# Performance work log

Measured on AMD Instinct MI355X. Metric: run time of the kernel, lower is better.

Reference implementation:

```python
import jax, jax.numpy as jnp
import numpy as np

DIM = 768
NUM_HEADS = 16
HEAD_DIM = DIM // NUM_HEADS  # 48
SCALE = 1.0 / np.sqrt(HEAD_DIM).astype(np.float32)


def setup_inputs() -> dict:
    key = jax.random.key(0)
    k1, k2, k3 = jax.random.split(key, 3)
    B, S = 4, 2048
    x = jax.random.normal(k1, (B, S, DIM), dtype=jnp.float32)
    # nn.Linear(dim, 3*dim, bias=False): weight stored transposed -> use [in, out]
    w_qkv = jax.random.normal(k2, (DIM, 3 * DIM), dtype=jnp.float32) * (1.0 / np.sqrt(DIM))
    w_proj = jax.random.normal(k3, (DIM, DIM), dtype=jnp.float32) * (1.0 / np.sqrt(DIM))
    b_proj = jnp.zeros((DIM,), dtype=jnp.float32)
    return {"x": x, "w_qkv": w_qkv, "w_proj": w_proj, "b_proj": b_proj}


def reference(x, w_qkv, w_proj, b_proj):
    B, S, D = x.shape
    qkv = x @ w_qkv                                   # [B,S,3D]
    qkv = qkv.reshape(B, S, 3, NUM_HEADS, HEAD_DIM)
    q, k, v = jnp.moveaxis(qkv, 2, 0)                 # each [B,S,H,hd]
    q = q.transpose(0, 2, 1, 3)                       # [B,H,S,hd]
    k = k.transpose(0, 2, 1, 3)
    v = v.transpose(0, 2, 1, 3)
    attn = jnp.einsum('bhqd,bhkd->bhqk', q, k) * SCALE
    attn = jax.nn.softmax(attn, axis=-1)              # dropout: identity (eval mode)
    out = jnp.einsum('bhqk,bhkd->bhqd', attn, v)      # [B,H,S,hd]
    out = out.transpose(0, 2, 1, 3).reshape(B, S, D)
    return out @ w_proj + b_proj
```

## Files before the change

kernel.cpp:

```cpp
#include <hip/hip_runtime.h>
#include <hip/hip_bf16.h>

#define DIMD   768
#define HEADS  16
#define HD     48
#define SEQ    2048
#define BATCH  4
#define NTOK   (BATCH * SEQ)
#define QKVD   (3 * DIMD)

typedef __attribute__((ext_vector_type(8)))  short s16x8;
typedef __attribute__((ext_vector_type(4)))  float f32x4;
typedef __attribute__((ext_vector_type(16))) float f32x16;
typedef unsigned short ushort_t;

static __device__ __forceinline__ unsigned short f2b(float f) {
  union { __hip_bfloat16 b; unsigned short s; } u;
  u.b = __float2bfloat16(f);
  return u.s;
}
static __device__ __forceinline__ float b2f(unsigned short v) {
  union { float f; unsigned u; } x;
  x.u = ((unsigned)v) << 16;
  return x.f;
}
static __device__ __forceinline__ unsigned pk2(float a, float b) {
  return (unsigned)f2b(a) | ((unsigned)f2b(b) << 16);
}

static __device__ __forceinline__ void gload_lds16(const void* g, void* l) {
  __builtin_amdgcn_global_load_lds(
      (const __attribute__((address_space(1))) unsigned int*)g,
      (__attribute__((address_space(3))) unsigned int*)l, 16, 0, 0);
}

__global__ __launch_bounds__(256) void cvt_bf16(const float* __restrict__ in,
                                                ushort_t* __restrict__ out, int n8) {
  int i = blockIdx.x * 256 + threadIdx.x;
  if (i >= n8) return;
  float4 a = ((const float4*)in)[i * 2];
  float4 b = ((const float4*)in)[i * 2 + 1];
  s16x8 v;
  v[0] = (short)f2b(a.x); v[1] = (short)f2b(a.y);
  v[2] = (short)f2b(a.z); v[3] = (short)f2b(a.w);
  v[4] = (short)f2b(b.x); v[5] = (short)f2b(b.y);
  v[6] = (short)f2b(b.z); v[7] = (short)f2b(b.w);
  ((s16x8*)out)[i] = v;
}

__global__ __launch_bounds__(256) void tcvt_bf16(const float* __restrict__ in,
                                                 ushort_t* __restrict__ out,
                                                 int R, int C) {
  __shared__ float T[32][33];
  const int c0 = blockIdx.x * 32, r0 = blockIdx.y * 32;
  const int lc = threadIdx.x & 31, lr = threadIdx.x >> 5;
#pragma unroll
  for (int i = 0; i < 4; ++i)
    T[lr + 8 * i][lc] = in[(size_t)(r0 + lr + 8 * i) * C + c0 + lc];
  __syncthreads();
#pragma unroll
  for (int i = 0; i < 4; ++i)
    out[(size_t)(c0 + lr + 8 * i) * R + r0 + lc] = f2b(T[lc][lr + 8 * i]);
}

template <int OUT_BF16>
__global__ __launch_bounds__(256) void gemm_bf16(
    const ushort_t* __restrict__ A, const ushort_t* __restrict__ Bt,
    const float* __restrict__ bias, void* __restrict__ Cout,
    int M, int N, int K) {
  __shared__ __align__(16) ushort_t As[128 * 64];
  __shared__ __align__(16) ushort_t Bs[128 * 64];

  const int tid = threadIdx.x;
  const int lane = tid & 63;
  const int w = tid >> 6;
  const int m0 = blockIdx.y * 128, n0 = blockIdx.x * 128;
  const int wm = (w >> 1) * 64, wn = (w & 1) * 64;

  const int c16s = (tid & 7) ^ ((tid >> 3) & 7);
  const ushort_t* aSrc = A + (size_t)(m0 + (tid >> 3)) * K + c16s * 8;
  const ushort_t* bSrc = Bt + (size_t)(n0 + (tid >> 3)) * K + c16s * 8;

  f32x4 acc[4][4];
#pragma unroll
  for (int i = 0; i < 4; ++i)
#pragma unroll
    for (int j = 0; j < 4; ++j) {
      acc[i][j][0] = 0.f; acc[i][j][1] = 0.f;
      acc[i][j][2] = 0.f; acc[i][j][3] = 0.f;
    }

  for (int k0 = 0; k0 < K; k0 += 64) {
    __syncthreads();
#pragma unroll
    for (int r = 0; r < 4; ++r) {
      gload_lds16(aSrc + (size_t)(r * 32) * K + k0,
                  (char*)As + (r * 256 + w * 64) * 16);
      gload_lds16(bSrc + (size_t)(r * 32) * K + k0,
                  (char*)Bs + (r * 256 + w * 64) * 16);
    }
    __syncthreads();

#pragma unroll
    for (int ks = 0; ks < 2; ++ks) {
      s16x8 af[4], bfr[4];
#pragma unroll
      for (int i = 0; i < 4; ++i) {
        const int ar = wm + i * 16 + (lane & 15);
        const int ac = (ks * 4 + (lane >> 4)) ^ (ar & 7);
        af[i] = *(const s16x8*)&As[ar * 64 + ac * 8];
        const int br = wn + i * 16 + (lane & 15);
        const int bc = (ks * 4 + (lane >> 4)) ^ (br & 7);
        bfr[i] = *(const s16x8*)&Bs[br * 64 + bc * 8];
      }
#pragma unroll
      for (int i = 0; i < 4; ++i)
#pragma unroll
        for (int j = 0; j < 4; ++j)
          acc[i][j] = __builtin_amdgcn_mfma_f32_16x16x32_bf16(
              af[i], bfr[j], acc[i][j], 0, 0, 0);
    }
  }

  if (OUT_BF16) {
    ushort_t* C = (ushort_t*)Cout;
#pragma unroll
    for (int i = 0; i < 4; ++i)
#pragma unroll
      for (int j = 0; j < 4; ++j) {
        const int col = n0 + wn + j * 16 + (lane & 15);
#pragma unroll
        for (int r = 0; r < 4; ++r) {
          const int row = m0 + wm + i * 16 + (lane >> 4) * 4 + r;
          C[(size_t)row * N + col] = f2b(acc[i][j][r]);
        }
      }
  } else {
    float* C = (float*)Cout;
#pragma unroll
    for (int i = 0; i < 4; ++i)
#pragma unroll
      for (int j = 0; j < 4; ++j) {
        const int col = n0 + wn + j * 16 + (lane & 15);
        const float bv = bias ? bias[col] : 0.f;
#pragma unroll
        for (int r = 0; r < 4; ++r) {
          const int row = m0 + wm + i * 16 + (lane >> 4) * 4 + r;
          C[(size_t)row * N + col] = acc[i][j][r] + bv;
        }
      }
  }
}

#define KVB 64
#define QPW 32
#define QPB 256
#define NT  (SEQ / KVB)

__global__ __launch_bounds__(512) void attn_mfma(const ushort_t* __restrict__ QKV,
                                                 ushort_t* __restrict__ Aout) {
  const int bh = blockIdx.x;
  const int qt = blockIdx.y;
  const int b = bh >> 4, h = bh & 15;
  const int tid  = threadIdx.x;
  const int w    = tid >> 6;
  const int lane = tid & 63;
  const int l31  = lane & 31;
  const int hi   = lane >> 5;

  __shared__ __align__(16) ushort_t Kfrag[6 * 64 * 8];
  __shared__ __align__(16) ushort_t Vt[64 * 64];

  if (tid < 240) *(uint2*)&Vt[49 * 64 + tid * 4] = make_uint2(0u, 0u);
  if (tid < 64) Vt[48 * 64 + tid] = (ushort_t)0x3F80;

  const ushort_t* qkv_b = QKV + (size_t)b * SEQ * QKVD;

  const float qs = 0.14433756729740643f * 1.44269504088896340f;
  const int qrow = qt * QPB + w * QPW + l31;
  const ushort_t* qsrc = qkv_b + (size_t)qrow * QKVD + h * HD;
  s16x8 qf[3];
#pragma unroll
  for (int ks = 0; ks < 3; ++ks) {
    s16x8 raw = *(const s16x8*)(qsrc + ks * 16 + hi * 8);
    s16x8 v;
#pragma unroll
    for (int j = 0; j < 8; ++j) v[j] = (short)f2b(b2f((unsigned short)raw[j]) * qs);
    qf[ks] = v;
  }

  f32x16 o[2];
#pragma unroll
  for (int mt = 0; mt < 2; ++mt)
#pragma unroll
    for (int r = 0; r < 16; ++r) o[mt][r] = 0.f;

  const int srow = lane;
  const int g0 = w;
  const ushort_t* kv0 = qkv_b + (size_t)srow * QKVD + DIMD + h * HD;

  s16x8 ka, va;
  auto loadKV = [&](int kt) {
    if (g0 < 6) {
      const ushort_t* base = kv0 + (size_t)(kt * KVB) * QKVD;
      ka = *(const s16x8*)(base + g0 * 8);
      va = *(const s16x8*)(base + DIMD + g0 * 8);
    }
  };
  auto writeKV = [&]() {
    if (g0 < 6) {
      const int slot = (srow >> 5) * 3 + (g0 >> 1);
      const int pos = (((srow & 31) + ((g0 & 1) << 5)) ^ slot);
      *(s16x8*)&Kfrag[(slot * 64 + pos) * 8] = ka;
#pragma unroll
      for (int j = 0; j < 8; ++j)
        Vt[(8 * g0 + j) * 64 + (srow ^ (j << 3))] = (ushort_t)va[j];
    }
  };

  loadKV(0);

  for (int kt = 0; kt < NT; ++kt) {
    __syncthreads();
    writeKV();
    __syncthreads();
    if (kt + 1 < NT) loadKV(kt + 1);

    f32x16 s0, s1;
#pragma unroll
    for (int r = 0; r < 16; ++r) { s0[r] = 0.f; s1[r] = 0.f; }
    __builtin_amdgcn_s_setprio(1);
#pragma unroll
    for (int ks = 0; ks < 3; ++ks) {
      s16x8 a0 = *(const s16x8*)&Kfrag[(ks * 64 + (lane ^ ks)) * 8];
      s0 = __builtin_amdgcn_mfma_f32_32x32x16_bf16(a0, qf[ks], s0, 0, 0, 0);
      s16x8 a1 = *(const s16x8*)&Kfrag[((3 + ks) * 64 + (lane ^ (3 + ks))) * 8];
      s1 = __builtin_amdgcn_mfma_f32_32x32x16_bf16(a1, qf[ks], s1, 0, 0, 0);
    }
    __builtin_amdgcn_s_setprio(0);

    unsigned pw0[8], pw1[8];
#pragma unroll
    for (int g = 0; g < 8; ++g) {
      pw0[g] = pk2(__builtin_amdgcn_exp2f(s0[2 * g]),
                   __builtin_amdgcn_exp2f(s0[2 * g + 1]));
      pw1[g] = pk2(__builtin_amdgcn_exp2f(s1[2 * g]),
                   __builtin_amdgcn_exp2f(s1[2 * g + 1]));
    }

    __builtin_amdgcn_s_setprio(1);
#pragma unroll
    for (int ks = 0; ks < 4; ++ks) {
      unsigned w0 = (ks < 2) ? pw0[4 * (ks & 1) + 0] : pw1[4 * (ks & 1) + 0];
      unsigned w1 = (ks < 2) ? pw0[4 * (ks & 1) + 1] : pw1[4 * (ks & 1) + 1];
      unsigned w2 = (ks < 2) ? pw0[4 * (ks & 1) + 2] : pw1[4 * (ks & 1) + 2];
      unsigned w3 = (ks < 2) ? pw0[4 * (ks & 1) + 3] : pw1[4 * (ks & 1) + 3];
      asm("v_permlane32_swap_b32 %0, %1" : "+v"(w0), "+v"(w2));
      asm("v_permlane32_swap_b32 %0, %1" : "+v"(w1), "+v"(w3));
      union { unsigned u[4]; s16x8 v; } pf;
      pf.u[0] = w0; pf.u[1] = w1; pf.u[2] = w2; pf.u[3] = w3;
      const int keyb = ks * 16 + hi * 8;
#pragma unroll
      for (int mt = 0; mt < 2; ++mt) {
        const int hd = mt * 32 + l31;
        s16x8 vfrag = *(const s16x8*)&Vt[hd * 64 + (keyb ^ ((hd & 7) << 3))];
        o[mt] = __builtin_amdgcn_mfma_f32_32x32x16_bf16(vfrag, pf.v, o[mt], 0, 0, 0);
      }
    }
    __builtin_amdgcn_s_setprio(0);
  }

  const float lsum = __shfl(o[1][8], l31, 64);
  const float inv = 1.f / lsum;
  const int token = qt * QPB + w * QPW + l31;
  ushort_t* dst = Aout + ((size_t)b * SEQ + token) * DIMD + h * HD;
#pragma unroll
  for (int rq = 0; rq < 4; ++rq) {
    const int hd0 = 8 * rq + 4 * hi;
    uint2 pk;
    pk.x = pk2(o[0][4 * rq + 0] * inv, o[0][4 * rq + 1] * inv);
    pk.y = pk2(o[0][4 * rq + 2] * inv, o[0][4 * rq + 3] * inv);
    *(uint2*)(dst + hd0) = pk;
  }
#pragma unroll
  for (int rq = 0; rq < 2; ++rq) {
    const int hd0 = 32 + 8 * rq + 4 * hi;
    uint2 pk;
    pk.x = pk2(o[1][4 * rq + 0] * inv, o[1][4 * rq + 1] * inv);
    pk.y = pk2(o[1][4 * rq + 2] * inv, o[1][4 * rq + 3] * inv);
    *(uint2*)(dst + hd0) = pk;
  }
}

extern "C" void kernel_launch(void* const* d_in, const int* in_sizes, int n_in,
                              void* d_out, int out_size, void* d_ws, size_t ws_size,
                              hipStream_t stream) {
  const float* x      = (const float*)d_in[0];
  const float* w_qkv  = (const float*)d_in[1];
  const float* w_proj = (const float*)d_in[2];
  const float* b_proj = (const float*)d_in[3];
  float* out = (float*)d_out;

  ushort_t* xb     = (ushort_t*)d_ws;
  ushort_t* wqkvT  = xb + (size_t)NTOK * DIMD;
  ushort_t* wprojT = wqkvT + (size_t)QKVD * DIMD;
  ushort_t* qkv    = wprojT + (size_t)DIMD * DIMD;
  ushort_t* att    = qkv + (size_t)NTOK * QKVD;

  cvt_bf16<<<(NTOK * DIMD / 8 + 255) / 256, 256, 0, stream>>>(x, xb, NTOK * DIMD / 8);
  tcvt_bf16<<<dim3(QKVD / 32, DIMD / 32), 256, 0, stream>>>(w_qkv, wqkvT, DIMD, QKVD);
  tcvt_bf16<<<dim3(DIMD / 32, DIMD / 32), 256, 0, stream>>>(w_proj, wprojT, DIMD, DIMD);

  gemm_bf16<1><<<dim3(QKVD / 128, NTOK / 128), 256, 0, stream>>>(
      xb, wqkvT, nullptr, qkv, NTOK, QKVD, DIMD);

  attn_mfma<<<dim3(BATCH * HEADS, SEQ / QPB), 512, 0, stream>>>(qkv, att);

  gemm_bf16<0><<<dim3(DIMD / 128, NTOK / 128), 256, 0, stream>>>(
      att, wprojT, b_proj, out, NTOK, DIMD, DIMD);
}
```

Baseline: 151.5 us.

## Split attention KV loop across two blocks and merge partials in a new kernel

The attention grid gains a third dimension that divides the key/value sequence into two halves, so twice as many blocks run concurrently. Each block writes unnormalized fp16 partial outputs and its row sums to workspace. A new merge kernel adds the two partials and divides by the combined sum before producing the bf16 attention output. This targets low occupancy in the attention kernel, at the cost of extra global traffic, one more launch, and the risk of fp16 overflow or precision loss in the unnormalized partials.

New measurement: 162.7 us. +7.5%, slower.

```diff
diff --git a/kernel.cpp b/kernel.cpp
--- a/kernel.cpp
+++ b/kernel.cpp
@@ -1,5 +1,6 @@
 #include <hip/hip_runtime.h>
 #include <hip/hip_bf16.h>
+#include <hip/hip_fp16.h>
 
 #define DIMD   768
 #define HEADS  16
@@ -26,6 +27,19 @@
 }
 static __device__ __forceinline__ unsigned pk2(float a, float b) {
   return (unsigned)f2b(a) | ((unsigned)f2b(b) << 16);
+}
+static __device__ __forceinline__ unsigned short f2h(float f) {
+  union { __half h; unsigned short s; } u;
+  u.h = __float2half(f);
+  return u.s;
+}
+static __device__ __forceinline__ float h2f(unsigned short s) {
+  union { __half h; unsigned short s; } u;
+  u.s = s;
+  return __half2float(u.h);
+}
+static __device__ __forceinline__ unsigned pk2h(float a, float b) {
+  return (unsigned)f2h(a) | ((unsigned)f2h(b) << 16);
 }
 
 static __device__ __forceinline__ void gload_lds16(const void* g, void* l) {
@@ -156,11 +170,14 @@
 #define QPW 32
 #define QPB 256
 #define NT  (SEQ / KVB)
+#define NTS (NT / 2)
 
 __global__ __launch_bounds__(512) void attn_mfma(const ushort_t* __restrict__ QKV,
-                                                 ushort_t* __restrict__ Aout) {
+                                                 ushort_t* __restrict__ Opart,
+                                                 float* __restrict__ Lpart) {
   const int bh = blockIdx.x;
   const int qt = blockIdx.y;
+  const int ks_split = blockIdx.z;
   const int b = bh >> 4, h = bh & 15;
   const int tid  = threadIdx.x;
   const int w    = tid >> 6;
@@ -218,13 +235,14 @@
     }
   };
 
-  loadKV(0);
-
-  for (int kt = 0; kt < NT; ++kt) {
+  const int kt0 = ks_split * NTS;
+  loadKV(kt0);
+
+  for (int it = 0; it < NTS; ++it) {
     __syncthreads();
     writeKV();
     __syncthreads();
-    if (kt + 1 < NT) loadKV(kt + 1);
+    if (it + 1 < NTS) loadKV(kt0 + it + 1);
 
     f32x16 s0, s1;
 #pragma unroll
@@ -270,26 +288,52 @@
     __builtin_amdgcn_s_setprio(0);
   }
 
-  const float lsum = __shfl(o[1][8], l31, 64);
-  const float inv = 1.f / lsum;
   const int token = qt * QPB + w * QPW + l31;
-  ushort_t* dst = Aout + ((size_t)b * SEQ + token) * DIMD + h * HD;
+  const size_t tokg = (size_t)ks_split * NTOK + (size_t)b * SEQ + token;
+  ushort_t* dst = Opart + tokg * DIMD + h * HD;
 #pragma unroll
   for (int rq = 0; rq < 4; ++rq) {
     const int hd0 = 8 * rq + 4 * hi;
     uint2 pk;
-    pk.x = pk2(o[0][4 * rq + 0] * inv, o[0][4 * rq + 1] * inv);
-    pk.y = pk2(o[0][4 * rq + 2] * inv, o[0][4 * rq + 3] * inv);
+    pk.x = pk2h(o[0][4 * rq + 0], o[0][4 * rq + 1]);
+    pk.y = pk2h(o[0][4 * rq + 2], o[0][4 * rq + 3]);
     *(uint2*)(dst + hd0) = pk;
   }
 #pragma unroll
   for (int rq = 0; rq < 2; ++rq) {
     const int hd0 = 32 + 8 * rq + 4 * hi;
     uint2 pk;
-    pk.x = pk2(o[1][4 * rq + 0] * inv, o[1][4 * rq + 1] * inv);
-    pk.y = pk2(o[1][4 * rq + 2] * inv, o[1][4 * rq + 3] * inv);
+    pk.x = pk2h(o[1][4 * rq + 0], o[1][4 * rq + 1]);
+    pk.y = pk2h(o[1][4 * rq + 2], o[1][4 * rq + 3]);
     *(uint2*)(dst + hd0) = pk;
   }
+  if (hi == 0) Lpart[tokg * HEADS + h] = o[1][8];
+}
+
+__global__ __launch_bounds__(256) void merge_norm(const ushort_t* __restrict__ Opart,
+                                                  const float* __restrict__ Lpart,
+                                                  ushort_t* __restrict__ att) {
+  const int gid = blockIdx.x * 256 + threadIdx.x;
+  const int tok = gid / (DIMD / 4);
+  const int c4  = gid - tok * (DIMD / 4);
+  const int col = c4 * 4;
+  const int h   = col / HD;
+
+  const uint2 a = ((const uint2*)Opart)[(size_t)tok * (DIMD / 4) + c4];
+  const uint2 c = ((const uint2*)Opart)[((size_t)NTOK + tok) * (DIMD / 4) + c4];
+  const float l = Lpart[(size_t)tok * HEADS + h] +
+                  Lpart[((size_t)NTOK + tok) * HEADS + h];
+  const float inv = 1.f / l;
+
+  const float o0 = h2f((unsigned short)(a.x & 0xffff)) + h2f((unsigned short)(c.x & 0xffff));
+  const float o1 = h2f((unsigned short)(a.x >> 16))    + h2f((unsigned short)(c.x >> 16));
+  const float o2 = h2f((unsigned short)(a.y & 0xffff)) + h2f((unsigned short)(c.y & 0xffff));
+  const float o3 = h2f((unsigned short)(a.y >> 16))    + h2f((unsigned short)(c.y >> 16));
+
+  uint2 pk;
+  pk.x = pk2(o0 * inv, o1 * inv);
+  pk.y = pk2(o2 * inv, o3 * inv);
+  ((uint2*)att)[(size_t)tok * (DIMD / 4) + c4] = pk;
 }
 
 extern "C" void kernel_launch(void* const* d_in, const int* in_sizes, int n_in,
@@ -306,6 +350,8 @@
   ushort_t* wprojT = wqkvT + (size_t)QKVD * DIMD;
   ushort_t* qkv    = wprojT + (size_t)DIMD * DIMD;
   ushort_t* att    = qkv + (size_t)NTOK * QKVD;
+  ushort_t* Opart  = att + (size_t)NTOK * DIMD;
+  float*    Lpart  = (float*)(Opart + (size_t)2 * NTOK * DIMD);
 
   cvt_bf16<<<(NTOK * DIMD / 8 + 255) / 256, 256, 0, stream>>>(x, xb, NTOK * DIMD / 8);
   tcvt_bf16<<<dim3(QKVD / 32, DIMD / 32), 256, 0, stream>>>(w_qkv, wqkvT, DIMD, QKVD);
@@ -314,7 +360,9 @@
   gemm_bf16<1><<<dim3(QKVD / 128, NTOK / 128), 256, 0, stream>>>(
       xb, wqkvT, nullptr, qkv, NTOK, QKVD, DIMD);
 
-  attn_mfma<<<dim3(BATCH * HEADS, SEQ / QPB), 512, 0, stream>>>(qkv, att);
+  attn_mfma<<<dim3(BATCH * HEADS, SEQ / QPB, 2), 512, 0, stream>>>(qkv, Opart, Lpart);
+
+  merge_norm<<<NTOK * DIMD / 4 / 256, 256, 0, stream>>>(Opart, Lpart, att);
 
   gemm_bf16<0><<<dim3(DIMD / 128, NTOK / 128), 256, 0, stream>>>(
       att, wprojT, b_proj, out, NTOK, DIMD, DIMD);
```

## Double KV tile size to 128 keys per barrier-synchronized iteration

Applied to the files above, without the earlier changes.

The attention kernel now stages 128 keys of K and V per loop iteration instead of 64, halving the number of __syncthreads pairs and spreading the global loads over all 8 warps (12 load slots across warps). Each iteration runs two 64-key sub-blocks of the QK^T/exp/PV MFMA pipeline from the larger shared-memory tiles. This is meant to cut barrier and load-latency overhead per key. In exchange it doubles LDS use and raises register pressure from the extra prefetch registers.

Measured after the change: 166.1 us. +9.7%, slower.

```diff
diff --git a/kernel.cpp b/kernel.cpp
--- a/kernel.cpp
+++ b/kernel.cpp
@@ -152,10 +152,9 @@
   }
 }
 
-#define KVB 64
 #define QPW 32
 #define QPB 256
-#define NT  (SEQ / KVB)
+#define NT2 (SEQ / 128)
 
 __global__ __launch_bounds__(512) void attn_mfma(const ushort_t* __restrict__ QKV,
                                                  ushort_t* __restrict__ Aout) {
@@ -168,11 +167,11 @@
   const int l31  = lane & 31;
   const int hi   = lane >> 5;
 
-  __shared__ __align__(16) ushort_t Kfrag[6 * 64 * 8];
-  __shared__ __align__(16) ushort_t Vt[64 * 64];
-
-  if (tid < 240) *(uint2*)&Vt[49 * 64 + tid * 4] = make_uint2(0u, 0u);
-  if (tid < 64) Vt[48 * 64 + tid] = (ushort_t)0x3F80;
+  __shared__ __align__(16) ushort_t Kfrag[12 * 64 * 8];
+  __shared__ __align__(16) ushort_t Vt[64 * 128];
+
+  if (tid < 480) *(uint2*)&Vt[49 * 128 + tid * 4] = make_uint2(0u, 0u);
+  if (tid < 128) Vt[48 * 128 + tid] = (ushort_t)0x3F80;
 
   const ushort_t* qkv_b = QKV + (size_t)b * SEQ * QKVD;
 
@@ -195,79 +194,99 @@
 #pragma unroll
     for (int r = 0; r < 16; ++r) o[mt][r] = 0.f;
 
-  const int srow = lane;
-  const int g0 = w;
-  const ushort_t* kv0 = qkv_b + (size_t)srow * QKVD + DIMD + h * HD;
-
-  s16x8 ka, va;
-  auto loadKV = [&](int kt) {
-    if (g0 < 6) {
-      const ushort_t* base = kv0 + (size_t)(kt * KVB) * QKVD;
-      ka = *(const s16x8*)(base + g0 * 8);
-      va = *(const s16x8*)(base + DIMD + g0 * 8);
+  const int halfA = (w >= 6) ? 1 : 0;
+  const int gA    = w - 6 * halfA;
+  const int keyA  = lane + 64 * halfA;
+  const int gB    = w + 2;
+  const int keyB  = lane + 64;
+
+  const ushort_t* kvA = qkv_b + (size_t)keyA * QKVD + DIMD + h * HD;
+  const ushort_t* kvB = qkv_b + (size_t)keyB * QKVD + DIMD + h * HD;
+
+  s16x8 ka, va, kb, vb;
+  auto loadKV = [&](int it) {
+    const size_t off = (size_t)(it * 128) * QKVD;
+    ka = *(const s16x8*)(kvA + off + gA * 8);
+    va = *(const s16x8*)(kvA + off + DIMD + gA * 8);
+    if (w < 4) {
+      kb = *(const s16x8*)(kvB + off + gB * 8);
+      vb = *(const s16x8*)(kvB + off + DIMD + gB * 8);
     }
   };
   auto writeKV = [&]() {
-    if (g0 < 6) {
-      const int slot = (srow >> 5) * 3 + (g0 >> 1);
-      const int pos = (((srow & 31) + ((g0 & 1) << 5)) ^ slot);
+    {
+      const int slot = (keyA >> 5) * 3 + (gA >> 1);
+      const int pos = (((keyA & 31) + ((gA & 1) << 5)) ^ slot);
       *(s16x8*)&Kfrag[(slot * 64 + pos) * 8] = ka;
 #pragma unroll
       for (int j = 0; j < 8; ++j)
-        Vt[(8 * g0 + j) * 64 + (srow ^ (j << 3))] = (ushort_t)va[j];
+        Vt[(8 * gA + j) * 128 + (keyA ^ (j << 3))] = (ushort_t)va[j];
+    }
+    if (w < 4) {
+      const int slot = (keyB >> 5) * 3 + (gB >> 1);
+      const int pos = (((keyB & 31) + ((gB & 1) << 5)) ^ slot);
+      *(s16x8*)&Kfrag[(slot * 64 + pos) * 8] = kb;
+#pragma unroll
+      for (int j = 0; j < 8; ++j)
+        Vt[(8 * gB + j) * 128 + (keyB ^ (j << 3))] = (ushort_t)vb[j];
     }
   };
 
   loadKV(0);
 
-  for (int kt = 0; kt < NT; ++kt) {
+  for (int it = 0; it < NT2; ++it) {
     __syncthreads();
     writeKV();
     __syncthreads();
-    if (kt + 1 < NT) loadKV(kt + 1);
-
-    f32x16 s0, s1;
-#pragma unroll
-    for (int r = 0; r < 16; ++r) { s0[r] = 0.f; s1[r] = 0.f; }
-    __builtin_amdgcn_s_setprio(1);
-#pragma unroll
-    for (int ks = 0; ks < 3; ++ks) {
-      s16x8 a0 = *(const s16x8*)&Kfrag[(ks * 64 + (lane ^ ks)) * 8];
-      s0 = __builtin_amdgcn_mfma_f32_32x32x16_bf16(a0, qf[ks], s0, 0, 0, 0);
-      s16x8 a1 = *(const s16x8*)&Kfrag[((3 + ks) * 64 + (lane ^ (3 + ks))) * 8];
-      s1 = __builtin_amdgcn_mfma_f32_32x32x16_bf16(a1, qf[ks], s1, 0, 0, 0);
-    }
-    __builtin_amdgcn_s_setprio(0);
-
-    unsigned pw0[8], pw1[8];
-#pragma unroll
-    for (int g = 0; g < 8; ++g) {
-      pw0[g] = pk2(__builtin_amdgcn_exp2f(s0[2 * g]),
-                   __builtin_amdgcn_exp2f(s0[2 * g + 1]));
-      pw1[g] = pk2(__builtin_amdgcn_exp2f(s1[2 * g]),
-                   __builtin_amdgcn_exp2f(s1[2 * g + 1]));
-    }
-
-    __builtin_amdgcn_s_setprio(1);
-#pragma unroll
-    for (int ks = 0; ks < 4; ++ks) {
-      unsigned w0 = (ks < 2) ? pw0[4 * (ks & 1) + 0] : pw1[4 * (ks & 1) + 0];
-      unsigned w1 = (ks < 2) ? pw0[4 * (ks & 1) + 1] : pw1[4 * (ks & 1) + 1];
-      unsigned w2 = (ks < 2) ? pw0[4 * (ks & 1) + 2] : pw1[4 * (ks & 1) + 2];
-      unsigned w3 = (ks < 2) ? pw0[4 * (ks & 1) + 3] : pw1[4 * (ks & 1) + 3];
-      asm("v_permlane32_swap_b32 %0, %1" : "+v"(w0), "+v"(w2));
-      asm("v_permlane32_swap_b32 %0, %1" : "+v"(w1), "+v"(w3));
-      union { unsigned u[4]; s16x8 v; } pf;
-      pf.u[0] = w0; pf.u[1] = w1; pf.u[2] = w2; pf.u[3] = w3;
-      const int keyb = ks * 16 + hi * 8;
-#pragma unroll
-      for (int mt = 0; mt < 2; ++mt) {
-        const int hd = mt * 32 + l31;
-        s16x8 vfrag = *(const s16x8*)&Vt[hd * 64 + (keyb ^ ((hd & 7) << 3))];
-        o[mt] = __builtin_amdgcn_mfma_f32_32x32x16_bf16(vfrag, pf.v, o[mt], 0, 0, 0);
-      }
-    }
-    __builtin_amdgcn_s_setprio(0);
+    if (it + 1 < NT2) loadKV(it + 1);
+
+#pragma unroll
+    for (int h2 = 0; h2 < 2; ++h2) {
+      f32x16 s0, s1;
+#pragma unroll
+      for (int r = 0; r < 16; ++r) { s0[r] = 0.f; s1[r] = 0.f; }
+      __builtin_amdgcn_s_setprio(1);
+#pragma unroll
+      for (int ks = 0; ks < 3; ++ks) {
+        const int sl0 = 6 * h2 + ks;
+        s16x8 a0 = *(const s16x8*)&Kfrag[(sl0 * 64 + (lane ^ sl0)) * 8];
+        s0 = __builtin_amdgcn_mfma_f32_32x32x16_bf16(a0, qf[ks], s0, 0, 0, 0);
+        const int sl1 = 6 * h2 + 3 + ks;
+        s16x8 a1 = *(const s16x8*)&Kfrag[(sl1 * 64 + (lane ^ sl1)) * 8];
+        s1 = __builtin_amdgcn_mfma_f32_32x32x16_bf16(a1, qf[ks], s1, 0, 0, 0);
+      }
+      __builtin_amdgcn_s_setprio(0);
+
+      unsigned pw0[8], pw1[8];
+#pragma unroll
+      for (int g = 0; g < 8; ++g) {
+        pw0[g] = pk2(__builtin_amdgcn_exp2f(s0[2 * g]),
+                     __builtin_amdgcn_exp2f(s0[2 * g + 1]));
+        pw1[g] = pk2(__builtin_amdgcn_exp2f(s1[2 * g]),
+                     __builtin_amdgcn_exp2f(s1[2 * g + 1]));
+      }
+
+      __builtin_amdgcn_s_setprio(1);
+#pragma unroll
+      for (int ks = 0; ks < 4; ++ks) {
+        unsigned w0 = (ks < 2) ? pw0[4 * (ks & 1) + 0] : pw1[4 * (ks & 1) + 0];
+        unsigned w1 = (ks < 2) ? pw0[4 * (ks & 1) + 1] : pw1[4 * (ks & 1) + 1];
+        unsigned w2 = (ks < 2) ? pw0[4 * (ks & 1) + 2] : pw1[4 * (ks & 1) + 2];
+        unsigned w3 = (ks < 2) ? pw0[4 * (ks & 1) + 3] : pw1[4 * (ks & 1) + 3];
+        asm("v_permlane32_swap_b32 %0, %1" : "+v"(w0), "+v"(w2));
+        asm("v_permlane32_swap_b32 %0, %1" : "+v"(w1), "+v"(w3));
+        union { unsigned u[4]; s16x8 v; } pf;
+        pf.u[0] = w0; pf.u[1] = w1; pf.u[2] = w2; pf.u[3] = w3;
+        const int keyb = h2 * 64 + ks * 16 + hi * 8;
+#pragma unroll
+        for (int mt = 0; mt < 2; ++mt) {
+          const int hd = mt * 32 + l31;
+          s16x8 vfrag = *(const s16x8*)&Vt[hd * 128 + (keyb ^ ((hd & 7) << 3))];
+          o[mt] = __builtin_amdgcn_mfma_f32_32x32x16_bf16(vfrag, pf.v, o[mt], 0, 0, 0);
+        }
+      }
+      __builtin_amdgcn_s_setprio(0);
+    }
   }
 
   const float lsum = __shfl(o[1][8], l31, 64);
```
